# Optimization experiments

Measured on AMD Instinct MI355X. Metric: run time of the kernel, lower is better.

The kernel has to match this reference:

```python
import jax, jax.numpy as jnp
import numpy as np

B, M, L, E, H = 64, 1, 4096, 4096, 64  # note: module requires M==1 and B==H
DK = E // H
EPS = 1e-8  # torch CosineSimilarity eps


def setup_inputs() -> dict:
    key = jax.random.key(0)
    ks = jax.random.split(key, 11)
    s_in = 1.0 / np.sqrt(L)
    s_e = 1.0 / np.sqrt(E)
    u = lambda k, shape, s: jax.random.uniform(k, shape, jnp.float32, -s, s)
    return {
        "q": jax.random.normal(ks[0], (B, M, L), jnp.float32),
        "k": jax.random.normal(ks[1], (B, M, L), jnp.float32),
        "v": jax.random.normal(ks[2], (B, M, L), jnp.float32),
        "Wq": u(ks[3], (L, E), s_in), "bq": u(ks[4], (E,), s_in),
        "Wk": u(ks[5], (L, E), s_in), "bk": u(ks[6], (E,), s_in),
        "Wv": u(ks[7], (L, E), s_in), "bv": u(ks[8], (E,), s_in),
        "Wo": u(ks[9], (E, E), s_e), "bo": u(ks[10], (E,), s_e),
    }


def reference(q, k, v, Wq, bq, Wk, bk, Wv, bv, Wo, bo):
    b = q.shape[0]
    # M == 1, so (B,1,L) -> (B,L); project and split into heads: (B,H,DK)
    qh = (q[:, 0, :] @ Wq + bq).reshape(b, H, DK)
    kh = (k[:, 0, :] @ Wk + bk).reshape(b, H, DK)
    vh = (v[:, 0, :] @ Wv + bv).reshape(b, H, DK)
    # cosine similarity over dk (dim=2): (B,H)
    num = jnp.sum(qh * kh, axis=-1)
    den = jnp.maximum(
        jnp.sqrt(jnp.sum(qh * qh, axis=-1)) * jnp.sqrt(jnp.sum(kh * kh, axis=-1)),
        EPS,
    )
    dist = jax.nn.softmax(num / den, axis=-1)  # softmax over heads, (B,H)
    # dropout is identity in eval mode.
    # torch.matmul((B,H), (B,H,DK)) broadcasts to (B, B, DK): out[i,j] = dist[j] @ v[i]
    attn = jnp.einsum('jh,bhd->bjd', dist, vh)  # (B, B, DK), valid since B == H
    attn = attn.reshape(b, E)
    return attn @ Wo + bo  # (B, E)
```

## Files before the change

kernel.cpp:

```cpp
#include <hip/hip_runtime.h>
#include <hip/hip_bf16.h>
#include <math.h>


#define TL 4096
#define NB 64
#define KSQ 4
#define KSO 8

typedef float f32x4 __attribute__((ext_vector_type(4)));
typedef short bf16x8 __attribute__((ext_vector_type(8)));
typedef unsigned int uint32;
typedef unsigned short u16;

union B8 { uint32 u[4]; bf16x8 v; };

#define GLOAD_LDS(g, l)                                                        \
  __builtin_amdgcn_global_load_lds(                                           \
      (const __attribute__((address_space(1))) void*)(g),                     \
      (__attribute__((address_space(3))) void*)(l), 16, 0, 0)

__device__ __forceinline__ void split_pair(float f0, float f1, uint32& hp,
                                           uint32& lp) {
  uint32 u0 = __float_as_uint(f0), u1 = __float_as_uint(f1);
  hp = (u0 >> 16) | (u1 & 0xffff0000u);
  float l0 = f0 - __uint_as_float(u0 & 0xffff0000u);
  float l1 = f1 - __uint_as_float(u1 & 0xffff0000u);
  lp = (__float_as_uint(l0) >> 16) | (__float_as_uint(l1) & 0xffff0000u);
}


struct Ptrs3 { const float* X[3]; u16* H[3]; u16* L[3]; };

__global__ __launch_bounds__(256) void prep_kernel(Ptrs3 p) {
  const int m = blockIdx.y;
  const int fid = blockIdx.x * 256 + threadIdx.x;
  const int lane = fid & 63, fi = fid >> 6;
  const int t = fi >> 2, rt = fi & 3;
  const int row = rt * 16 + (lane & 15);
  const int k0 = t * 32 + (lane >> 4) * 8;
  const float* src = p.X[m] + (size_t)row * TL + k0;
  const float4 f0 = *reinterpret_cast<const float4*>(src);
  const float4 f1 = *reinterpret_cast<const float4*>(src + 4);
  uint4 h, l;
  split_pair(f0.x, f0.y, h.x, l.x);
  split_pair(f0.z, f0.w, h.y, l.y);
  split_pair(f1.x, f1.y, h.z, l.z);
  split_pair(f1.z, f1.w, h.w, l.w);
  *reinterpret_cast<uint4*>(p.H[m] + (size_t)fid * 8) = h;
  *reinterpret_cast<uint4*>(p.L[m] + (size_t)fid * 8) = l;
}

struct GemmArgs {
  const u16* Ah[3];
  const u16* Al[3];
  const float* W[3];
  float* P[3];
};

template <int KSplit, int NMat>
__global__ __launch_bounds__(256, 3) void mfma_gemm(GemmArgs ga) {
  constexpr int KR = TL / KSplit;
  constexpr int NT = KR / 32;
  constexpr int NWG = NMat * KSplit * 64;
  constexpr int TSZ = 16384;
  static_assert(NWG % 8 == 0, "xcd swizzle needs NWG%8==0");
  static_assert(NT >= 2, "pipeline needs >=2 tiles");
  __shared__ __align__(16) char sb[3 * TSZ];

  const int tid = threadIdx.x;
  const int lane = tid & 63;
  const int w = tid >> 6;
  const int l15 = lane & 15, kg = lane >> 4;

  const int swz = (blockIdx.x & 7) * (NWG / 8) + (blockIdx.x >> 3);
  const int mat = swz / (KSplit * 64);
  const int r = swz % (KSplit * 64);
  const int ks = r >> 6;
  const int ct = r & 63;
  const int k0 = ks * KR;
  const int tg0 = ks * NT;
  const int colg0 = ct * 64;

  const float* Wm = ga.W[mat];
  const u16* Agh = ga.Ah[mat];
  const u16* Agl = ga.Al[mat];

  const int half = w >> 1;
  const int part = w & 1;
  const u16* Abase = (half ? Agl : Agh) + (size_t)part * 1024 + lane * 8;
  char* const adst0 = sb + 8192 + half * 4096 + part * 2048;

  auto STAGE = [&](char* buf, int t) {
    const int kb = k0 + t * 32;
#pragma unroll
    for (int i = 0; i < 2; ++i) {
      const int krow = w * 8 + i * 4 + (lane >> 4);
      const float* gsrc = Wm + (size_t)(kb + krow) * TL + colg0 + (lane & 15) * 4;
      GLOAD_LDS(gsrc, buf + (w * 8 + i * 4) * 256);
    }
    const u16* asrc = Abase + (size_t)(tg0 + t) * 2048;
    char* adst = (buf - sb) + adst0;
    GLOAD_LDS(asrc, adst);
    GLOAD_LDS(asrc + 512, adst + 1024);
  };

  f32x4 acc[4] = {};

  auto COMPUTE = [&](const char* buf) {
    const float* Bf = (const float*)buf;
    const char* Ahb = buf + 8192;
    const char* Alb = buf + 12288;
    float f[8];
#pragma unroll
    for (int e = 0; e < 8; ++e) f[e] = Bf[(kg * 8 + e) * 64 + w * 16 + l15];
    B8 bh, bl;
#pragma unroll
    for (int e = 0; e < 4; ++e)
      split_pair(f[2 * e], f[2 * e + 1], bh.u[e], bl.u[e]);
#pragma unroll
    for (int rt = 0; rt < 4; ++rt) {
      const bf16x8 ah = *(const bf16x8*)(Ahb + rt * 1024 + lane * 16);
      const bf16x8 al = *(const bf16x8*)(Alb + rt * 1024 + lane * 16);
      acc[rt] = __builtin_amdgcn_mfma_f32_16x16x32_bf16(ah, bh.v, acc[rt], 0, 0, 0);
      acc[rt] = __builtin_amdgcn_mfma_f32_16x16x32_bf16(ah, bl.v, acc[rt], 0, 0, 0);
      acc[rt] = __builtin_amdgcn_mfma_f32_16x16x32_bf16(al, bh.v, acc[rt], 0, 0, 0);
    }
  };

  STAGE(sb, 0);
  STAGE(sb + TSZ, 1);

#pragma unroll 1
  for (int t = 0; t < NT; ++t) {
    char* cur = sb + (t % 3) * TSZ;
    if (t + 2 < NT) {
      STAGE(sb + ((t + 2) % 3) * TSZ, t + 2);
      asm volatile("s_waitcnt vmcnt(8)" ::: "memory");
    } else if (t + 2 == NT) {
      asm volatile("s_waitcnt vmcnt(4)" ::: "memory");
    } else {
      asm volatile("s_waitcnt vmcnt(0)" ::: "memory");
    }
    __builtin_amdgcn_s_barrier();
    COMPUTE(cur);
    __builtin_amdgcn_s_barrier();
  }

  float* Pp = ga.P[mat] + ((size_t)ks * NB) * TL + colg0 + w * 16 + l15;
#pragma unroll
  for (int rt = 0; rt < 4; ++rt)
#pragma unroll
    for (int j = 0; j < 4; ++j)
      Pp[(size_t)(rt * 16 + kg * 4 + j) * TL] = acc[rt][j];
}

__global__ __launch_bounds__(64) void dist_kernel(
    const float* __restrict__ Pq, const float* __restrict__ Pk,
    const float* __restrict__ bq, const float* __restrict__ bk,
    float* __restrict__ dist) {
  const int b = blockIdx.x;
  const int h = threadIdx.x;
  float num = 0.f, qq = 0.f, kk = 0.f;
#pragma unroll
  for (int d = 0; d < 64; d += 4) {
    f32x4 qv = *(const f32x4*)&bq[h * 64 + d];
    f32x4 kv = *(const f32x4*)&bk[h * 64 + d];
#pragma unroll
    for (int s = 0; s < KSQ; ++s) {
      qv += *(const f32x4*)&Pq[((size_t)s * NB + b) * TL + h * 64 + d];
      kv += *(const f32x4*)&Pk[((size_t)s * NB + b) * TL + h * 64 + d];
    }
#pragma unroll
    for (int e = 0; e < 4; ++e) {
      num += qv[e] * kv[e];
      qq += qv[e] * qv[e];
      kk += kv[e] * kv[e];
    }
  }
  const float den = fmaxf(sqrtf(qq) * sqrtf(kk), 1e-8f);
  float s = num / den;
  float m = s;
#pragma unroll
  for (int off = 32; off; off >>= 1) m = fmaxf(m, __shfl_xor(m, off));
  const float e = expf(s - m);
  float sum = e;
#pragma unroll
  for (int off = 32; off; off >>= 1) sum += __shfl_xor(sum, off);
  dist[b * 64 + h] = e / sum;
}

__global__ __launch_bounds__(256) void attn_kernel(
    const float* __restrict__ Pv, const float* __restrict__ bv,
    const float* __restrict__ dist, u16* __restrict__ Ah,
    u16* __restrict__ Al) {
  const int i = blockIdx.x;
  __shared__ float vrow[TL];
  __shared__ float ds[NB * NB];
  const int tid = threadIdx.x;
#pragma unroll
  for (int f = tid; f < 1024; f += 256) {
    f32x4 v = *(const f32x4*)&bv[f * 4];
#pragma unroll
    for (int s = 0; s < KSQ; ++s)
      v += *(const f32x4*)&Pv[((size_t)s * NB + i) * TL + f * 4];
    *reinterpret_cast<f32x4*>(&vrow[f * 4]) = v;
    *reinterpret_cast<f32x4*>(&ds[f * 4]) =
        *reinterpret_cast<const f32x4*>(&dist[f * 4]);
  }
  __syncthreads();
  const int rt = i >> 4, l15r = i & 15;
#pragma unroll
  for (int s = 0; s < 16; ++s) {
    const int c = tid + 256 * s;
    const int j = c >> 6, d = c & 63;
    float sum = 0.f;
#pragma unroll
    for (int h = 0; h < 64; ++h) sum += ds[j * 64 + h] * vrow[h * 64 + d];
    const uint32 u = __float_as_uint(sum);
    const float lo = sum - __uint_as_float(u & 0xffff0000u);
    const uint32 off =
        (((uint32)(c >> 5) * 4 + rt) * 64 + ((c >> 3) & 3) * 16 + l15r) * 8 +
        (c & 7);
    Ah[off] = (u16)(u >> 16);
    Al[off] = (u16)(__float_as_uint(lo) >> 16);
  }
}

__global__ __launch_bounds__(256) void reduce_kernel(
    const float* __restrict__ Po, const float* __restrict__ bo,
    float* __restrict__ out) {
  const int idx = (blockIdx.x * 256 + threadIdx.x) * 4;
  f32x4 v = *(const f32x4*)&bo[idx & (TL - 1)];
#pragma unroll
  for (int s = 0; s < KSO; ++s)
    v += *(const f32x4*)&Po[(size_t)s * NB * TL + idx];
  *reinterpret_cast<f32x4*>(&out[idx]) = v;
}

extern "C" void kernel_launch(void* const* d_in, const int* in_sizes, int n_in,
                              void* d_out, int out_size, void* d_ws,
                              size_t ws_size, hipStream_t stream) {
  const float* q  = (const float*)d_in[0];
  const float* k  = (const float*)d_in[1];
  const float* v  = (const float*)d_in[2];
  const float* Wq = (const float*)d_in[3];
  const float* bq = (const float*)d_in[4];
  const float* Wk = (const float*)d_in[5];
  const float* bk = (const float*)d_in[6];
  const float* Wv = (const float*)d_in[7];
  const float* bv = (const float*)d_in[8];
  const float* Wo = (const float*)d_in[9];
  const float* bo = (const float*)d_in[10];
  float* out = (float*)d_out;

  char* ws = (char*)d_ws;
  const size_t HB = 512u * 1024u;
  u16* qAh = (u16*)(ws + 0 * HB);
  u16* qAl = (u16*)(ws + 1 * HB);
  u16* kAh = (u16*)(ws + 2 * HB);
  u16* kAl = (u16*)(ws + 3 * HB);
  u16* vAh = (u16*)(ws + 4 * HB);
  u16* vAl = (u16*)(ws + 5 * HB);
  u16* aAh = (u16*)(ws + 6 * HB);
  u16* aAl = (u16*)(ws + 7 * HB);
  float* Pq = (float*)(ws + (4u << 20));
  float* Pk = (float*)(ws + (8u << 20));
  float* Pv = (float*)(ws + (12u << 20));
  float* Po = Pq;
  float* dist = (float*)(ws + (16u << 20));

  Ptrs3 p3;
  p3.X[0] = q; p3.X[1] = k; p3.X[2] = v;
  p3.H[0] = qAh; p3.H[1] = kAh; p3.H[2] = vAh;
  p3.L[0] = qAl; p3.L[1] = kAl; p3.L[2] = vAl;
  prep_kernel<<<dim3(128, 3), 256, 0, stream>>>(p3);

  GemmArgs gq;
  gq.Ah[0] = qAh; gq.Ah[1] = kAh; gq.Ah[2] = vAh;
  gq.Al[0] = qAl; gq.Al[1] = kAl; gq.Al[2] = vAl;
  gq.W[0] = Wq; gq.W[1] = Wk; gq.W[2] = Wv;
  gq.P[0] = Pq; gq.P[1] = Pk; gq.P[2] = Pv;
  mfma_gemm<KSQ, 3><<<3 * KSQ * 64, 256, 0, stream>>>(gq);

  dist_kernel<<<NB, 64, 0, stream>>>(Pq, Pk, bq, bk, dist);

  attn_kernel<<<NB, 256, 0, stream>>>(Pv, bv, dist, aAh, aAl);

  GemmArgs go;
  go.Ah[0] = aAh; go.Ah[1] = aAh; go.Ah[2] = aAh;
  go.Al[0] = aAl; go.Al[1] = aAl; go.Al[2] = aAl;
  go.W[0] = Wo; go.W[1] = Wo; go.W[2] = Wo;
  go.P[0] = Po; go.P[1] = Po; go.P[2] = Po;
  mfma_gemm<KSO, 1><<<KSO * 64, 256, 0, stream>>>(go);

  reduce_kernel<<<256, 256, 0, stream>>>(Po, bo, out);
}
```

Baseline: 113.2 us.

## Widen GEMM column tiles with 8-wave workgroups sharing staged activation tiles

The split-bf16 MFMA GEMM now uses 512-thread workgroups covering 256 (QKV) or 128 (output) columns instead of 64. The staged bf16 hi/lo activation fragments are loaded into registers once per k-step and reused across several column subtiles. Buffer rotation now swaps pointers instead of using modulo indexing. The aim is to cut redundant activation staging and per-workgroup overhead. The cost is far fewer workgroups (192 and 256), which lowers parallelism and increases LDS and register pressure per workgroup.

```diff
diff --git a/kernel.cpp b/kernel.cpp
--- a/kernel.cpp
+++ b/kernel.cpp
@@ -19,6 +19,8 @@
   __builtin_amdgcn_global_load_lds(                                           \
       (const __attribute__((address_space(1))) void*)(g),                     \
       (__attribute__((address_space(3))) void*)(l), 16, 0, 0)
+
+#define WAITCNT(n) asm volatile("s_waitcnt vmcnt(" #n ")" ::: "memory")
 
 __device__ __forceinline__ void split_pair(float f0, float f1, uint32& hp,
                                            uint32& lp) {
@@ -58,14 +60,19 @@
   float* P[3];
 };
 
-template <int KSplit, int NMat>
-__global__ __launch_bounds__(256, 3) void mfma_gemm(GemmArgs ga) {
+template <int KSplit, int NMat, int CB>
+__global__ __launch_bounds__(512, 2) void mfma_gemm(GemmArgs ga) {
   constexpr int KR = TL / KSplit;
   constexpr int NT = KR / 32;
-  constexpr int NWG = NMat * KSplit * 64;
-  constexpr int TSZ = 16384;
+  constexpr int NCG = TL / CB;
+  constexpr int NWG = NMat * KSplit * NCG;
+  constexpr int BSZ = CB * 128;
+  constexpr int TSZ = BSZ + 8192;
+  constexpr int NBG = CB / 64;
+  constexpr int LPR = CB / 4;
+  constexpr int SUB = CB / 128;
   static_assert(NWG % 8 == 0, "xcd swizzle needs NWG%8==0");
-  static_assert(NT >= 2, "pipeline needs >=2 tiles");
+  static_assert(NT >= 3, "pipeline needs >=3 tiles");
   __shared__ __align__(16) char sb[3 * TSZ];
 
   const int tid = threadIdx.x;
@@ -74,85 +81,94 @@
   const int l15 = lane & 15, kg = lane >> 4;
 
   const int swz = (blockIdx.x & 7) * (NWG / 8) + (blockIdx.x >> 3);
-  const int mat = swz / (KSplit * 64);
-  const int r = swz % (KSplit * 64);
-  const int ks = r >> 6;
-  const int ct = r & 63;
+  const int mat = swz / (KSplit * NCG);
+  const int r = swz % (KSplit * NCG);
+  const int ks = r / NCG;
+  const int cg = r % NCG;
   const int k0 = ks * KR;
   const int tg0 = ks * NT;
-  const int colg0 = ct * 64;
+  const int cg0 = cg * CB;
 
   const float* Wm = ga.W[mat];
   const u16* Agh = ga.Ah[mat];
   const u16* Agl = ga.Al[mat];
 
-  const int half = w >> 1;
-  const int part = w & 1;
-  const u16* Abase = (half ? Agl : Agh) + (size_t)part * 1024 + lane * 8;
-  char* const adst0 = sb + 8192 + half * 4096 + part * 2048;
+  const u16* Asrc0 = (w < 4 ? Agh : Agl) + (size_t)(w & 3) * 512 + lane * 8;
+  const int adst = BSZ + (w < 4 ? 0 : 4096) + (w & 3) * 1024;
 
   auto STAGE = [&](char* buf, int t) {
     const int kb = k0 + t * 32;
 #pragma unroll
-    for (int i = 0; i < 2; ++i) {
-      const int krow = w * 8 + i * 4 + (lane >> 4);
-      const float* gsrc = Wm + (size_t)(kb + krow) * TL + colg0 + (lane & 15) * 4;
-      GLOAD_LDS(gsrc, buf + (w * 8 + i * 4) * 256);
-    }
-    const u16* asrc = Abase + (size_t)(tg0 + t) * 2048;
-    char* adst = (buf - sb) + adst0;
-    GLOAD_LDS(asrc, adst);
-    GLOAD_LDS(asrc + 512, adst + 1024);
+    for (int i = 0; i < NBG; ++i) {
+      const int gl = w * NBG + i;
+      const float* gsrc = Wm + (size_t)(kb + gl * (64 / LPR) + lane / LPR) * TL +
+                          cg0 + (lane % LPR) * 4;
+      GLOAD_LDS(gsrc, buf + gl * 1024);
+    }
+    GLOAD_LDS(Asrc0 + (size_t)(tg0 + t) * 2048, buf + adst);
   };
 
-  f32x4 acc[4] = {};
+  f32x4 acc[SUB][4] = {};
 
   auto COMPUTE = [&](const char* buf) {
     const float* Bf = (const float*)buf;
-    const char* Ahb = buf + 8192;
-    const char* Alb = buf + 12288;
-    float f[8];
-#pragma unroll
-    for (int e = 0; e < 8; ++e) f[e] = Bf[(kg * 8 + e) * 64 + w * 16 + l15];
-    B8 bh, bl;
-#pragma unroll
-    for (int e = 0; e < 4; ++e)
-      split_pair(f[2 * e], f[2 * e + 1], bh.u[e], bl.u[e]);
+    const char* Ahb = buf + BSZ;
+    const char* Alb = buf + BSZ + 4096;
+    bf16x8 ah[4], al[4];
 #pragma unroll
     for (int rt = 0; rt < 4; ++rt) {
-      const bf16x8 ah = *(const bf16x8*)(Ahb + rt * 1024 + lane * 16);
-      const bf16x8 al = *(const bf16x8*)(Alb + rt * 1024 + lane * 16);
-      acc[rt] = __builtin_amdgcn_mfma_f32_16x16x32_bf16(ah, bh.v, acc[rt], 0, 0, 0);
-      acc[rt] = __builtin_amdgcn_mfma_f32_16x16x32_bf16(ah, bl.v, acc[rt], 0, 0, 0);
-      acc[rt] = __builtin_amdgcn_mfma_f32_16x16x32_bf16(al, bh.v, acc[rt], 0, 0, 0);
+      ah[rt] = *(const bf16x8*)(Ahb + rt * 1024 + lane * 16);
+      al[rt] = *(const bf16x8*)(Alb + rt * 1024 + lane * 16);
+    }
+#pragma unroll
+    for (int c2 = 0; c2 < SUB; ++c2) {
+      const int wcol = w * (CB / 8) + c2 * 16;
+      float f[8];
+#pragma unroll
+      for (int e = 0; e < 8; ++e) f[e] = Bf[(kg * 8 + e) * CB + wcol + l15];
+      B8 bh, bl;
+#pragma unroll
+      for (int e = 0; e < 4; ++e)
+        split_pair(f[2 * e], f[2 * e + 1], bh.u[e], bl.u[e]);
+#pragma unroll
+      for (int rt = 0; rt < 4; ++rt) {
+        acc[c2][rt] = __builtin_amdgcn_mfma_f32_16x16x32_bf16(ah[rt], bh.v, acc[c2][rt], 0, 0, 0);
+        acc[c2][rt] = __builtin_amdgcn_mfma_f32_16x16x32_bf16(ah[rt], bl.v, acc[c2][rt], 0, 0, 0);
+        acc[c2][rt] = __builtin_amdgcn_mfma_f32_16x16x32_bf16(al[rt], bh.v, acc[c2][rt], 0, 0, 0);
+      }
     }
   };
 
-  STAGE(sb, 0);
-  STAGE(sb + TSZ, 1);
+  char* cur = sb;
+  char* nxt = sb + TSZ;
+  char* stg = sb + 2 * TSZ;
+  STAGE(cur, 0);
+  STAGE(nxt, 1);
 
 #pragma unroll 1
   for (int t = 0; t < NT; ++t) {
-    char* cur = sb + (t % 3) * TSZ;
     if (t + 2 < NT) {
-      STAGE(sb + ((t + 2) % 3) * TSZ, t + 2);
-      asm volatile("s_waitcnt vmcnt(8)" ::: "memory");
+      STAGE(stg, t + 2);
+      if constexpr (NBG == 4) WAITCNT(10); else WAITCNT(6);
     } else if (t + 2 == NT) {
-      asm volatile("s_waitcnt vmcnt(4)" ::: "memory");
+      if constexpr (NBG == 4) WAITCNT(5); else WAITCNT(3);
     } else {
-      asm volatile("s_waitcnt vmcnt(0)" ::: "memory");
+      WAITCNT(0);
     }
     __builtin_amdgcn_s_barrier();
     COMPUTE(cur);
     __builtin_amdgcn_s_barrier();
+    char* tmp = cur; cur = nxt; nxt = stg; stg = tmp;
   }
 
-  float* Pp = ga.P[mat] + ((size_t)ks * NB) * TL + colg0 + w * 16 + l15;
-#pragma unroll
-  for (int rt = 0; rt < 4; ++rt)
-#pragma unroll
-    for (int j = 0; j < 4; ++j)
-      Pp[(size_t)(rt * 16 + kg * 4 + j) * TL] = acc[rt][j];
+  float* Pp = ga.P[mat] + ((size_t)ks * NB) * TL + cg0 + w * (CB / 8) + l15;
+#pragma unroll
+  for (int c2 = 0; c2 < SUB; ++c2)
+#pragma unroll
+    for (int rt = 0; rt < 4; ++rt)
+#pragma unroll
+      for (int j = 0; j < 4; ++j)
+        Pp[(size_t)(rt * 16 + kg * 4 + j) * TL + c2 * 16] = acc[c2][rt][j];
 }
 
 __global__ __launch_bounds__(64) void dist_kernel(
@@ -281,7 +297,7 @@
   gq.Al[0] = qAl; gq.Al[1] = kAl; gq.Al[2] = vAl;
   gq.W[0] = Wq; gq.W[1] = Wk; gq.W[2] = Wv;
   gq.P[0] = Pq; gq.P[1] = Pk; gq.P[2] = Pv;
-  mfma_gemm<KSQ, 3><<<3 * KSQ * 64, 256, 0, stream>>>(gq);
+  mfma_gemm<KSQ, 3, 256><<<3 * KSQ * 16, 512, 0, stream>>>(gq);
 
   dist_kernel<<<NB, 64, 0, stream>>>(Pq, Pk, bq, bk, dist);
 
@@ -292,7 +308,7 @@
   go.Al[0] = aAl; go.Al[1] = aAl; go.Al[2] = aAl;
   go.W[0] = Wo; go.W[1] = Wo; go.W[2] = Wo;
   go.P[0] = Po; go.P[1] = Po; go.P[2] = Po;
-  mfma_gemm<KSO, 1><<<KSO * 64, 256, 0, stream>>>(go);
+  mfma_gemm<KSO, 1, 128><<<KSO * 32, 512, 0, stream>>>(go);
 
   reduce_kernel<<<256, 256, 0, stream>>>(Po, bo, out);
 }
```

After: 105.4 us. 1.07x faster.

## Deepen GEMM prefetch pipeline to four stages and raise QKV split-K when workspace allows

Applied to the files above, without the earlier changes.

The mfma_gemm LDS ring grows from 3 to 5 tile buffers, so four tiles are in flight instead of two, with the vmcnt waits adjusted to match. Launch bounds drop from 3 to 2 blocks per CU to fit the larger shared memory. When the workspace is at least 30 MiB, the QKV projection uses split-K 8 instead of 4, giving more workgroups, and the partial buffers are relocated to fit. The downstream reduction loops take the split count at runtime, which costs their unrolling. The aim is to hide more weight-streaming latency in this memory-bound GEMM, at the price of occupancy and extra partial-sum traffic.

```diff
diff --git a/kernel.cpp b/kernel.cpp
--- a/kernel.cpp
+++ b/kernel.cpp
@@ -5,8 +5,6 @@
 
 #define TL 4096
 #define NB 64
-#define KSQ 4
-#define KSO 8
 
 typedef float f32x4 __attribute__((ext_vector_type(4)));
 typedef short bf16x8 __attribute__((ext_vector_type(8)));
@@ -19,6 +17,8 @@
   __builtin_amdgcn_global_load_lds(                                           \
       (const __attribute__((address_space(1))) void*)(g),                     \
       (__attribute__((address_space(3))) void*)(l), 16, 0, 0)
+
+#define WAITCNT(n) asm volatile("s_waitcnt vmcnt(" #n ")" ::: "memory")
 
 __device__ __forceinline__ void split_pair(float f0, float f1, uint32& hp,
                                            uint32& lp) {
@@ -59,14 +59,14 @@
 };
 
 template <int KSplit, int NMat>
-__global__ __launch_bounds__(256, 3) void mfma_gemm(GemmArgs ga) {
+__global__ __launch_bounds__(256, 2) void mfma_gemm(GemmArgs ga) {
   constexpr int KR = TL / KSplit;
   constexpr int NT = KR / 32;
   constexpr int NWG = NMat * KSplit * 64;
   constexpr int TSZ = 16384;
   static_assert(NWG % 8 == 0, "xcd swizzle needs NWG%8==0");
-  static_assert(NT >= 2, "pipeline needs >=2 tiles");
-  __shared__ __align__(16) char sb[3 * TSZ];
+  static_assert(NT >= 6, "depth-4 pipeline needs >=6 tiles");
+  __shared__ __align__(16) char sb[5 * TSZ];
 
   const int tid = threadIdx.x;
   const int lane = tid & 63;
@@ -89,7 +89,7 @@
   const int half = w >> 1;
   const int part = w & 1;
   const u16* Abase = (half ? Agl : Agh) + (size_t)part * 1024 + lane * 8;
-  char* const adst0 = sb + 8192 + half * 4096 + part * 2048;
+  const int adst0 = 8192 + half * 4096 + part * 2048;
 
   auto STAGE = [&](char* buf, int t) {
     const int kb = k0 + t * 32;
@@ -100,7 +100,7 @@
       GLOAD_LDS(gsrc, buf + (w * 8 + i * 4) * 256);
     }
     const u16* asrc = Abase + (size_t)(tg0 + t) * 2048;
-    char* adst = (buf - sb) + adst0;
+    char* adst = buf + adst0;
     GLOAD_LDS(asrc, adst);
     GLOAD_LDS(asrc + 512, adst + 1024);
   };
@@ -128,23 +128,32 @@
     }
   };
 
-  STAGE(sb, 0);
-  STAGE(sb + TSZ, 1);
-
+  STAGE(sb + 0 * TSZ, 0);
+  STAGE(sb + 1 * TSZ, 1);
+  STAGE(sb + 2 * TSZ, 2);
+  STAGE(sb + 3 * TSZ, 3);
+
+  int cb = 0;
+  int sn = 4;
 #pragma unroll 1
   for (int t = 0; t < NT; ++t) {
-    char* cur = sb + (t % 3) * TSZ;
-    if (t + 2 < NT) {
-      STAGE(sb + ((t + 2) % 3) * TSZ, t + 2);
-      asm volatile("s_waitcnt vmcnt(8)" ::: "memory");
+    if (t + 4 < NT) {
+      STAGE(sb + sn * TSZ, t + 4);
+      WAITCNT(16);
+    } else if (t + 4 == NT) {
+      WAITCNT(12);
+    } else if (t + 3 == NT) {
+      WAITCNT(8);
     } else if (t + 2 == NT) {
-      asm volatile("s_waitcnt vmcnt(4)" ::: "memory");
+      WAITCNT(4);
     } else {
-      asm volatile("s_waitcnt vmcnt(0)" ::: "memory");
+      WAITCNT(0);
     }
     __builtin_amdgcn_s_barrier();
-    COMPUTE(cur);
+    COMPUTE(sb + cb * TSZ);
     __builtin_amdgcn_s_barrier();
+    cb = (cb == 4) ? 0 : cb + 1;
+    sn = (sn == 4) ? 0 : sn + 1;
   }
 
   float* Pp = ga.P[mat] + ((size_t)ks * NB) * TL + colg0 + w * 16 + l15;
@@ -158,7 +167,7 @@
 __global__ __launch_bounds__(64) void dist_kernel(
     const float* __restrict__ Pq, const float* __restrict__ Pk,
     const float* __restrict__ bq, const float* __restrict__ bk,
-    float* __restrict__ dist) {
+    float* __restrict__ dist, int nks) {
   const int b = blockIdx.x;
   const int h = threadIdx.x;
   float num = 0.f, qq = 0.f, kk = 0.f;
@@ -166,8 +175,7 @@
   for (int d = 0; d < 64; d += 4) {
     f32x4 qv = *(const f32x4*)&bq[h * 64 + d];
     f32x4 kv = *(const f32x4*)&bk[h * 64 + d];
-#pragma unroll
-    for (int s = 0; s < KSQ; ++s) {
+    for (int s = 0; s < nks; ++s) {
       qv += *(const f32x4*)&Pq[((size_t)s * NB + b) * TL + h * 64 + d];
       kv += *(const f32x4*)&Pk[((size_t)s * NB + b) * TL + h * 64 + d];
     }
@@ -193,7 +201,7 @@
 __global__ __launch_bounds__(256) void attn_kernel(
     const float* __restrict__ Pv, const float* __restrict__ bv,
     const float* __restrict__ dist, u16* __restrict__ Ah,
-    u16* __restrict__ Al) {
+    u16* __restrict__ Al, int nks) {
   const int i = blockIdx.x;
   __shared__ float vrow[TL];
   __shared__ float ds[NB * NB];
@@ -201,8 +209,7 @@
 #pragma unroll
   for (int f = tid; f < 1024; f += 256) {
     f32x4 v = *(const f32x4*)&bv[f * 4];
-#pragma unroll
-    for (int s = 0; s < KSQ; ++s)
+    for (int s = 0; s < nks; ++s)
       v += *(const f32x4*)&Pv[((size_t)s * NB + i) * TL + f * 4];
     *reinterpret_cast<f32x4*>(&vrow[f * 4]) = v;
     *reinterpret_cast<f32x4*>(&ds[f * 4]) =
@@ -229,11 +236,10 @@
 
 __global__ __launch_bounds__(256) void reduce_kernel(
     const float* __restrict__ Po, const float* __restrict__ bo,
-    float* __restrict__ out) {
+    float* __restrict__ out, int nks) {
   const int idx = (blockIdx.x * 256 + threadIdx.x) * 4;
   f32x4 v = *(const f32x4*)&bo[idx & (TL - 1)];
-#pragma unroll
-  for (int s = 0; s < KSO; ++s)
+  for (int s = 0; s < nks; ++s)
     v += *(const f32x4*)&Po[(size_t)s * NB * TL + idx];
   *reinterpret_cast<f32x4*>(&out[idx]) = v;
 }
@@ -264,11 +270,13 @@
   u16* vAl = (u16*)(ws + 5 * HB);
   u16* aAh = (u16*)(ws + 6 * HB);
   u16* aAl = (u16*)(ws + 7 * HB);
-  float* Pq = (float*)(ws + (4u << 20));
-  float* Pk = (float*)(ws + (8u << 20));
-  float* Pv = (float*)(ws + (12u << 20));
+
+  const bool big = ws_size >= ((size_t)30 << 20);
+  float* Pq = (float*)(ws + ((size_t)4 << 20));
+  float* Pk = (float*)(ws + ((size_t)(big ? 12 : 8) << 20));
+  float* Pv = (float*)(ws + ((size_t)(big ? 20 : 12) << 20));
+  float* dist = (float*)(ws + ((size_t)(big ? 28 : 16) << 20));
   float* Po = Pq;
-  float* dist = (float*)(ws + (16u << 20));
 
   Ptrs3 p3;
   p3.X[0] = q; p3.X[1] = k; p3.X[2] = v;
@@ -281,18 +289,21 @@
   gq.Al[0] = qAl; gq.Al[1] = kAl; gq.Al[2] = vAl;
   gq.W[0] = Wq; gq.W[1] = Wk; gq.W[2] = Wv;
   gq.P[0] = Pq; gq.P[1] = Pk; gq.P[2] = Pv;
-  mfma_gemm<KSQ, 3><<<3 * KSQ * 64, 256, 0, stream>>>(gq);
-
-  dist_kernel<<<NB, 64, 0, stream>>>(Pq, Pk, bq, bk, dist);
-
-  attn_kernel<<<NB, 256, 0, stream>>>(Pv, bv, dist, aAh, aAl);
+  if (big)
+    mfma_gemm<8, 3><<<3 * 8 * 64, 256, 0, stream>>>(gq);
+  else
+    mfma_gemm<4, 3><<<3 * 4 * 64, 256, 0, stream>>>(gq);
+
+  dist_kernel<<<NB, 64, 0, stream>>>(Pq, Pk, bq, bk, dist, big ? 8 : 4);
+
+  attn_kernel<<<NB, 256, 0, stream>>>(Pv, bv, dist, aAh, aAl, big ? 8 : 4);
 
   GemmArgs go;
   go.Ah[0] = aAh; go.Ah[1] = aAh; go.Ah[2] = aAh;
   go.Al[0] = aAl; go.Al[1] = aAl; go.Al[2] = aAl;
   go.W[0] = Wo; go.W[1] = Wo; go.W[2] = Wo;
   go.P[0] = Po; go.P[1] = Po; go.P[2] = Po;
-  mfma_gemm<KSO, 1><<<KSO * 64, 256, 0, stream>>>(go);
-
-  reduce_kernel<<<256, 256, 0, stream>>>(Po, bo, out);
-}
+  mfma_gemm<8, 1><<<8 * 64, 256, 0, stream>>>(go);
+
+  reduce_kernel<<<256, 256, 0, stream>>>(Po, bo, out, 8);
+}
```

After: 145.9 us. +28.8%, slower.
